# Kernel optimization log

Measured on AMD Instinct MI355X. Metric: run time of the kernel, lower is better.

## Reference

```python
import jax, jax.numpy as jnp
import numpy as np

B, T, D = 2, 2048, 1024
H = 16
HD = D // H
WINDOW = 128
N_GLOBAL = 1
SCALE = 1.0 / np.sqrt(HD)


def _attend_mask(T):
    # True = allowed to attend: banded local window + global rows/cols
    idx = jnp.arange(T)
    dist = jnp.abs(idx[:, None] - idx[None, :])
    attend = dist <= WINDOW
    glb = idx < N_GLOBAL
    attend = attend | glb[:, None] | glb[None, :]
    return attend  # [T, T] bool


def setup_inputs() -> dict:
    key = jax.random.key(0)
    ks = jax.random.split(key, 5)
    scale_w = 1.0 / np.sqrt(D)
    return {
        "x": jax.random.normal(ks[0], (B, T, D), dtype=jnp.float32),
        "Wq": jax.random.normal(ks[1], (D, D), dtype=jnp.float32) * scale_w,
        "Wk": jax.random.normal(ks[2], (D, D), dtype=jnp.float32) * scale_w,
        "Wv": jax.random.normal(ks[3], (D, D), dtype=jnp.float32) * scale_w,
        "Wo": jax.random.normal(ks[4], (D, D), dtype=jnp.float32) * scale_w,
    }


def reference(x, Wq, Wk, Wv, Wo):
    Bb, Tt, Dd = x.shape
    # torch nn.Linear: y = x @ W.T
    q = (x @ Wq.T).reshape(Bb, Tt, H, HD).transpose(0, 2, 1, 3)  # [B,H,T,hd]
    k = (x @ Wk.T).reshape(Bb, Tt, H, HD).transpose(0, 2, 1, 3)
    v = (x @ Wv.T).reshape(Bb, Tt, H, HD).transpose(0, 2, 1, 3)

    attend = _attend_mask(Tt)  # [T,T]
    logits = jnp.einsum("bhqd,bhkd->bhqk", q, k) * SCALE
    logits = jnp.where(attend[None, None, :, :], logits, -jnp.inf)
    weights = jax.nn.softmax(logits, axis=-1)
    weights = jnp.nan_to_num(weights)
    out = jnp.einsum("bhqk,bhkd->bhqd", weights, v)
    out = out.transpose(0, 2, 1, 3).reshape(Bb, Tt, Dd)
    return out @ Wo.T
```

## Files before the change

kernel.cpp:

```cpp
#include <hip/hip_runtime.h>

typedef unsigned short u16;
typedef __attribute__((ext_vector_type(8))) __bf16 bf16x8;
typedef __attribute__((ext_vector_type(4))) float f32x4;
typedef __attribute__((ext_vector_type(8))) u16 u16x8;

#define T_SEQ 2048
#define DIM   1024
#define HDIM  64
#define WIN   128
#define XN_EL (2 * T_SEQ * DIM)

#define AS1 __attribute__((address_space(1)))
#define AS3 __attribute__((address_space(3)))

__device__ __forceinline__ u16 f2bf(float f) {
  union { float f; unsigned u; } v; v.f = f;
  unsigned r = v.u + 0x7fffu + ((v.u >> 16) & 1u);
  return (u16)(r >> 16);
}
__device__ __forceinline__ float bf2f(u16 u) {
  union { unsigned u; float f; } v; v.u = ((unsigned)u) << 16; return v.f;
}
__device__ __forceinline__ void bar() {
  asm volatile("" ::: "memory");
  __builtin_amdgcn_s_barrier();
  asm volatile("" ::: "memory");
}

__global__ __launch_bounds__(256) void cvt_all(
    const float* __restrict__ x,  const float* __restrict__ wq,
    const float* __restrict__ wk, const float* __restrict__ wv,
    const float* __restrict__ wo, u16* __restrict__ xb, u16* __restrict__ wb) {
  const int bid = blockIdx.x;
  const float* s;
  u16* d;
  int off;
  if (bid < 2048) {
    s = x; d = xb; off = bid * 2048;
  } else {
    const int w = bid - 2048;
    const int m = w >> 9;
    s = (m == 0) ? wq : ((m == 1) ? wk : ((m == 2) ? wv : wo));
    d = wb + ((size_t)m << 20);
    off = (w & 511) * 2048;
  }
  const int i = off + threadIdx.x * 8;
  const float4* s4 = (const float4*)(s + i);
  float4 a = s4[0], b = s4[1];
  u16x8 r;
  r[0] = f2bf(a.x); r[1] = f2bf(a.y); r[2] = f2bf(a.z); r[3] = f2bf(a.w);
  r[4] = f2bf(b.x); r[5] = f2bf(b.y); r[6] = f2bf(b.z); r[7] = f2bf(b.w);
  *(u16x8*)(d + i) = r;
}

__global__ __launch_bounds__(512, 2) void gemm8(
    const u16* __restrict__ A, const u16* __restrict__ B,
    u16* __restrict__ C, int nbm) {
  constexpr int NT = 16;
  __shared__ u16 As[2][256 * 64];
  __shared__ u16 Bs[2][192 * 64];

  const int tid = threadIdx.x;
  const int lane = tid & 63;
  const int wid = tid >> 6;
  const int wr = wid >> 2, wc = wid & 3;
  const int c15 = lane & 15, g = lane >> 4;
  const int lr = lane >> 3;
  const int lcs = ((lane & 7) ^ lr) << 3;

  const int cpx = gridDim.x >> 3;
  const int bid = ((int)blockIdx.x & 7) * cpx + ((int)blockIdx.x >> 3);
  const int bm = bid % nbm;
  const int nb = bid / nbm;
  const u16* Ab = A + (size_t)bm * 256 * DIM;
  const u16* Bb = B + (size_t)nb * 192 * DIM;

  f32x4 acc[8][3];
#pragma unroll
  for (int m = 0; m < 8; ++m)
#pragma unroll
    for (int n = 0; n < 3; ++n) acc[m][n] = (f32x4){0.f, 0.f, 0.f, 0.f};

  auto stAh = [&](int buf, int half, int t) {
    const int k0 = t * 64;
#pragma unroll
    for (int i = 0; i < 2; ++i) {
      const int c = half * 16 + wid * 2 + i;
      __builtin_amdgcn_global_load_lds(
          (const AS1 void*)(Ab + (size_t)(c * 8 + lr) * DIM + k0 + lcs),
          (AS3 void*)(&As[buf][c * 512]), 16, 0, 0);
    }
  };
  auto stBt = [&](int buf, int third, int t) {
    const int k0 = t * 64;
    const int c = third * 8 + wid;
    __builtin_amdgcn_global_load_lds(
        (const AS1 void*)(Bb + (size_t)(c * 8 + lr) * DIM + k0 + lcs),
        (AS3 void*)(&Bs[buf][c * 512]), 16, 0, 0);
  };

  stAh(0, 0, 0); stAh(0, 1, 0);
  stBt(0, 0, 0); stBt(0, 1, 0); stBt(0, 2, 0);
  stBt(1, 0, 1); stBt(1, 1, 1); stBt(1, 2, 1);
  asm volatile("s_waitcnt vmcnt(3)" ::: "memory");
  bar();

  for (int t2 = 0; t2 < NT; t2 += 2) {
    bf16x8 bfrag[3][2];
#pragma unroll
    for (int p = 0; p < 8; ++p) {
      const int q = p & 3;
      const int buf = (p >> 2);
      if (q == 0) {
#pragma unroll
        for (int n = 0; n < 3; ++n)
#pragma unroll
          for (int ks = 0; ks < 2; ++ks) {
            const int r = wc * 48 + n * 16 + c15;
            bfrag[n][ks] = *(const bf16x8*)(
                &Bs[buf][r * 64 + ((ks * 32 + g * 8) ^ ((r & 7) << 3))]);
          }
      }
      bf16x8 af[2][2];
#pragma unroll
      for (int m = 0; m < 2; ++m)
#pragma unroll
        for (int ks = 0; ks < 2; ++ks) {
          const int r = wr * 128 + (q * 2 + m) * 16 + c15;
          af[m][ks] = *(const bf16x8*)(
              &As[buf][r * 64 + ((ks * 32 + g * 8) ^ ((r & 7) << 3))]);
        }
      const bool s2 = (t2 + 2) < NT;
      const bool s3 = (t2 + 3) < NT;
      if (p == 0) {
        stAh(1, 0, t2 + 1);
      } else if (p == 1) {
        stAh(1, 1, t2 + 1);
        if (s2) stBt(0, 0, t2 + 2);
      } else if (p == 2) {
        if (s2) stBt(0, 1, t2 + 2);
      } else if (p == 3) {
        if (s2) { stBt(0, 2, t2 + 2);
                  asm volatile("s_waitcnt vmcnt(3)" ::: "memory"); }
        else    { asm volatile("s_waitcnt vmcnt(0)" ::: "memory"); }
      } else if (p == 4) {
        if (s2) stAh(0, 0, t2 + 2);
      } else if (p == 5) {
        if (s2) stAh(0, 1, t2 + 2);
        if (s3) stBt(1, 0, t2 + 3);
      } else if (p == 6) {
        if (s3) stBt(1, 1, t2 + 3);
      } else {
        if (s3) { stBt(1, 2, t2 + 3);
                  asm volatile("s_waitcnt vmcnt(3)" ::: "memory"); }
        else if (s2) { asm volatile("s_waitcnt vmcnt(0)" ::: "memory"); }
      }
      bar();
      __builtin_amdgcn_s_setprio(1);
#pragma unroll
      for (int m = 0; m < 2; ++m)
#pragma unroll
        for (int n = 0; n < 3; ++n)
#pragma unroll
          for (int ks = 0; ks < 2; ++ks)
            acc[q * 2 + m][n] = __builtin_amdgcn_mfma_f32_16x16x32_bf16(
                af[m][ks], bfrag[n][ks], acc[q * 2 + m][n], 0, 0, 0);
      __builtin_amdgcn_s_setprio(0);
      bar();
    }
  }

#pragma unroll
  for (int m = 0; m < 8; ++m) {
    const int row0 = bm * 256 + wr * 128 + m * 16 + g * 4;
#pragma unroll
    for (int n = 0; n < 3; ++n) {
      const int col = nb * 192 + wc * 48 + n * 16 + c15;
#pragma unroll
      for (int j = 0; j < 4; ++j) {
        u16* dst = C + (size_t)(col >> 10) * (size_t)XN_EL +
                   (col & 1023) + (size_t)(row0 + j) * DIM;
        *dst = f2bf(acc[m][n][j]);
      }
    }
  }
}

template <int BM, int BN, int WM, int WN, int OS, typename OUT_T>
__global__ __launch_bounds__(WM * WN * 64, 2) void gemm3(
    const u16* __restrict__ A, const u16* __restrict__ B,
    OUT_T* __restrict__ C, int nbm) {
  constexpr int NW = WM * WN;
  constexpr int RM = BM / WM, RN = BN / WN;
  constexpr int MF = RM / 16, NF = RN / 16;
  constexpr int MPH = MF / 4;
  constexpr int NT = DIM / 64;
  constexpr int CA = BM / 8, CB = BN / 8;
  constexpr int ANW = CA / NW;
  constexpr int BNW = CB / NW;

  __shared__ u16 As[2][BM * 64];
  __shared__ u16 Bs[2][BN * 64];

  const int tid = threadIdx.x;
  const int lane = tid & 63;
  const int wid = tid >> 6;
  const int wr = wid / WN, wc = wid % WN;
  const int c15 = lane & 15, g = lane >> 4;
  const int lr = lane >> 3;
  const int lcs = ((lane & 7) ^ lr) << 3;

  const int cpx = gridDim.x >> 3;
  const int bid = ((int)blockIdx.x & 7) * cpx + ((int)blockIdx.x >> 3);
  const int bm = bid % nbm;
  const int nb = bid / nbm;
  const u16* Ab = A + (size_t)bm * BM * DIM;
  const u16* Bb = B + (size_t)nb * BN * DIM;

  f32x4 acc[MF][NF];
#pragma unroll
  for (int m = 0; m < MF; ++m)
#pragma unroll
    for (int n = 0; n < NF; ++n) acc[m][n] = (f32x4){0.f, 0.f, 0.f, 0.f};

  auto stA = [&](int buf, int half, int k0) {
#pragma unroll
    for (int i = 0; i < ANW / 2; ++i) {
      const int c = half * (CA / 2) + wid * (ANW / 2) + i;
      __builtin_amdgcn_global_load_lds(
          (const AS1 void*)(Ab + (size_t)(c * 8 + lr) * DIM + k0 + lcs),
          (AS3 void*)(&As[buf][c * 512]), 16, 0, 0);
    }
  };
  auto stB = [&](int buf, int k0) {
#pragma unroll
    for (int i = 0; i < BNW; ++i) {
      const int c = wid * BNW + i;
      __builtin_amdgcn_global_load_lds(
          (const AS1 void*)(Bb + (size_t)(c * 8 + lr) * DIM + k0 + lcs),
          (AS3 void*)(&Bs[buf][c * 512]), 16, 0, 0);
    }
  };

  stA(0, 0, 0); stA(0, 1, 0);
  stB(0, 0); stB(1, 64);
  asm volatile("s_waitcnt vmcnt(4)" ::: "memory");
  bar();

  for (int t = 0; t < NT; ++t) {
    const int buf = t & 1;
    const int k0 = t * 64;
    bf16x8 bfrag[NF][2];
#pragma unroll
    for (int p = 0; p < 4; ++p) {
      if (p == 0) {
#pragma unroll
        for (int n = 0; n < NF; ++n)
#pragma unroll
          for (int ks = 0; ks < 2; ++ks) {
            const int r = wc * RN + n * 16 + c15;
            bfrag[n][ks] = *(const bf16x8*)(
                &Bs[buf][r * 64 + ((ks * 32 + g * 8) ^ ((r & 7) << 3))]);
          }
      }
      bf16x8 af[MPH][2];
#pragma unroll
      for (int m = 0; m < MPH; ++m)
#pragma unroll
        for (int ks = 0; ks < 2; ++ks) {
          const int r = wr * RM + (p * MPH + m) * 16 + c15;
          af[m][ks] = *(const bf16x8*)(
              &As[buf][r * 64 + ((ks * 32 + g * 8) ^ ((r & 7) << 3))]);
        }
      if (p == 0) {
        if (t + 1 < NT) stA(buf ^ 1, 0, k0 + 64);
      } else if (p == 1) {
        if (t + 1 < NT) stA(buf ^ 1, 1, k0 + 64);
      } else if (p == 2) {
        if (t + 2 < NT) stB(buf, k0 + 128);
      } else {
        if (t < NT - 2) asm volatile("s_waitcnt vmcnt(4)" ::: "memory");
        else            asm volatile("s_waitcnt vmcnt(0)" ::: "memory");
      }
      bar();
      __builtin_amdgcn_s_setprio(1);
#pragma unroll
      for (int m = 0; m < MPH; ++m)
#pragma unroll
        for (int n = 0; n < NF; ++n)
#pragma unroll
          for (int ks = 0; ks < 2; ++ks)
            acc[p * MPH + m][n] = __builtin_amdgcn_mfma_f32_16x16x32_bf16(
                af[m][ks], bfrag[n][ks], acc[p * MPH + m][n], 0, 0, 0);
      __builtin_amdgcn_s_setprio(0);
      bar();
    }
  }

#pragma unroll
  for (int m = 0; m < MF; ++m) {
    const int row0 = bm * BM + wr * RM + m * 16 + g * 4;
#pragma unroll
    for (int n = 0; n < NF; ++n) {
      const int col = nb * BN + wc * RN + n * 16 + c15;
#pragma unroll
      for (int j = 0; j < 4; ++j) {
        const size_t idx = (size_t)(row0 + j) * OS + col;
        if constexpr (sizeof(OUT_T) == 2) C[idx] = f2bf(acc[m][n][j]);
        else C[idx] = acc[m][n][j];
      }
    }
  }
}

__global__ __launch_bounds__(256) void sparse_attn(
    const u16* __restrict__ Q, const u16* __restrict__ K,
    const u16* __restrict__ V, u16* __restrict__ AO) {
  __shared__ u16 Ks[64 * 72];
  __shared__ u16 Vt[64 * 72];
  __shared__ u16 Pl[4][16 * 72];
  __shared__ float Pg[4][32];

  const int tid = threadIdx.x;
  const int lane = tid & 63;
  const int wid = tid >> 6;
  const size_t ha = (size_t)blockIdx.z * T_SEQ * DIM + (size_t)blockIdx.y * HDIM;
  const u16* Qp = Q + ha;
  const u16* Kp = K + ha;
  const u16* Vp = V + ha;

  if (blockIdx.x == 16) {
    float* qs   = (float*)(&Pl[0][0]);
    float* ps   = (float*)Ks;
    float* rbuf = (float*)Vt;
    float* red  = (float*)Pg;

    if (tid < HDIM) qs[tid] = bf2f(Qp[tid]);
    __syncthreads();

    float lsum = 0.f;
#pragma unroll
    for (int j = 0; j < 8; ++j) {
      const int k = tid + 256 * j;
      const u16* kr = Kp + (size_t)k * DIM;
      float acc = 0.f;
#pragma unroll
      for (int d0 = 0; d0 < 8; ++d0) {
        u16x8 kv = *(const u16x8*)(kr + d0 * 8);
#pragma unroll
        for (int e = 0; e < 8; ++e) acc += qs[d0 * 8 + e] * bf2f(kv[e]);
      }
      const float p = __expf(acc * 0.125f);
      ps[k] = p;
      lsum += p;
    }
#pragma unroll
    for (int s = 1; s < 64; s <<= 1) lsum += __shfl_xor(lsum, s);
    if (lane == 0) red[wid] = lsum;
    __syncthreads();
    const float denom = red[0] + red[1] + red[2] + red[3];

    const int kg = tid >> 3, dg = tid & 7;
    float facc[8] = {0.f, 0.f, 0.f, 0.f, 0.f, 0.f, 0.f, 0.f};
#pragma unroll 8
    for (int i = 0; i < 64; ++i) {
      const int k = kg * 64 + i;
      const u16x8 vv = *(const u16x8*)(Vp + (size_t)k * DIM + dg * 8);
      const float p = ps[k];
#pragma unroll
      for (int e = 0; e < 8; ++e) facc[e] += p * bf2f(vv[e]);
    }
#pragma unroll
    for (int e = 0; e < 8; ++e) rbuf[kg * 64 + dg * 8 + e] = facc[e];
    __syncthreads();
    if (tid < HDIM) {
      float tot = 0.f;
#pragma unroll
      for (int k2 = 0; k2 < 32; ++k2) tot += rbuf[k2 * 64 + tid];
      AO[ha + tid] = f2bf(tot / denom);
    }
    return;
  }

  const int c15 = lane & 15;
  const int g = lane >> 4;
  const int q0 = blockIdx.x * 128;
  const int qw = q0 + wid * 32;

  bf16x8 qA0, qA1, qB0, qB1;
  {
    const u16* qp = Qp + (size_t)(qw + c15) * DIM + g * 8;
    qA0 = *(const bf16x8*)qp;
    qA1 = *(const bf16x8*)(qp + 32);
    const u16* qp2 = qp + 16 * DIM;
    qB0 = *(const bf16x8*)qp2;
    qB1 = *(const bf16x8*)(qp2 + 32);
  }

  float lrA[4] = {0.f, 0.f, 0.f, 0.f}, lrB[4] = {0.f, 0.f, 0.f, 0.f};
  f32x4 aoA[4], aoB[4];
#pragma unroll
  for (int c = 0; c < 4; ++c) {
    aoA[c] = (f32x4){0.f, 0.f, 0.f, 0.f};
    aoB[c] = (f32x4){0.f, 0.f, 0.f, 0.f};
  }

  const int klo = (q0 > WIN) ? (q0 - WIN) : 0;
  int khi = q0 + 128 + WIN;
  if (khi > T_SEQ) khi = T_SEQ;
  const int nt = (khi - klo) >> 6;

  const int srr = tid >> 2;
  const int scc = (tid & 3) * 16;
  const int vr = srr ^ (scc & 48);

  const u16* kbase = Kp + (size_t)(klo + srr) * DIM + scc;
  const u16* vbase = Vp + (size_t)(klo + srr) * DIM + scc;
  u16x8 kp0 = *(const u16x8*)kbase;
  u16x8 kp1 = *(const u16x8*)(kbase + 8);
  u16x8 vp0 = *(const u16x8*)vbase;
  u16x8 vp1 = *(const u16x8*)(vbase + 8);

  for (int ti = 0; ti < nt; ++ti) {
    const int kt = klo + ti * 64;
    *(u16x8*)(Ks + srr * 72 + scc) = kp0;
    *(u16x8*)(Ks + srr * 72 + scc + 8) = kp1;
#pragma unroll
    for (int e = 0; e < 8; ++e) {
      Vt[(scc + e) * 72 + vr] = vp0[e];
      Vt[(scc + 8 + e) * 72 + vr] = vp1[e];
    }
    __syncthreads();

    if (ti + 1 < nt) {
      const u16* kn = kbase + (size_t)(ti + 1) * 64 * DIM;
      const u16* vn = vbase + (size_t)(ti + 1) * 64 * DIM;
      kp0 = *(const u16x8*)kn;
      kp1 = *(const u16x8*)(kn + 8);
      vp0 = *(const u16x8*)vn;
      vp1 = *(const u16x8*)(vn + 8);
    }

    auto do_group = [&](const bf16x8& qf0, const bf16x8& qf1, int r0,
                        float* lrun, f32x4* ao) {
      f32x4 s[4];
#pragma unroll
      for (int t = 0; t < 4; ++t) {
        const u16* kr = Ks + (t * 16 + c15) * 72 + g * 8;
        bf16x8 ka = *(const bf16x8*)kr;
        bf16x8 kb = *(const bf16x8*)(kr + 32);
        f32x4 z = (f32x4){0.f, 0.f, 0.f, 0.f};
        z = __builtin_amdgcn_mfma_f32_16x16x32_bf16(qf0, ka, z, 0, 0, 0);
        s[t] = __builtin_amdgcn_mfma_f32_16x16x32_bf16(qf1, kb, z, 0, 0, 0);
      }
      if (kt >= r0 - 113 && kt <= r0 + 65) {
#pragma unroll
        for (int j = 0; j < 4; ++j) {
#pragma unroll
          for (int t = 0; t < 4; ++t) {
            const float p = __expf(s[t][j] * 0.125f);
            lrun[j] += p;
            Pl[wid][(g * 4 + j) * 72 + t * 16 + c15] = f2bf(p);
          }
        }
      } else {
#pragma unroll
        for (int j = 0; j < 4; ++j) {
          const int qg = r0 + g * 4 + j;
#pragma unroll
          for (int t = 0; t < 4; ++t) {
            const int kg = kt + t * 16 + c15;
            const int dd = qg - kg;
            const bool ok = (kg == 0) || (dd <= WIN && dd >= -WIN);
            const float p = ok ? __expf(s[t][j] * 0.125f) : 0.f;
            lrun[j] += p;
            Pl[wid][(g * 4 + j) * 72 + t * 16 + c15] = f2bf(p);
          }
        }
      }
      asm volatile("s_waitcnt lgkmcnt(0)" ::: "memory");

      const bf16x8 pa0 = *(const bf16x8*)(&Pl[wid][c15 * 72 + g * 8]);
      const bf16x8 pa1 = *(const bf16x8*)(&Pl[wid][c15 * 72 + 32 + g * 8]);
#pragma unroll
      for (int c = 0; c < 4; ++c) {
        const int rb = (c * 16 + c15) * 72;
        bf16x8 va = *(const bf16x8*)(Vt + rb + ((g * 8) ^ (c << 4)));
        bf16x8 vb = *(const bf16x8*)(Vt + rb + ((32 + g * 8) ^ (c << 4)));
        ao[c] = __builtin_amdgcn_mfma_f32_16x16x32_bf16(pa0, va, ao[c], 0, 0, 0);
        ao[c] = __builtin_amdgcn_mfma_f32_16x16x32_bf16(pa1, vb, ao[c], 0, 0, 0);
      }
    };

    do_group(qA0, qA1, qw, lrA, aoA);
    do_group(qB0, qB1, qw + 16, lrB, aoB);

    __syncthreads();
  }

  float ltA[4], ltB[4];
#pragma unroll
  for (int j = 0; j < 4; ++j) {
    float a = lrA[j], b = lrB[j];
    a += __shfl_xor(a, 1); b += __shfl_xor(b, 1);
    a += __shfl_xor(a, 2); b += __shfl_xor(b, 2);
    a += __shfl_xor(a, 4); b += __shfl_xor(b, 4);
    a += __shfl_xor(a, 8); b += __shfl_xor(b, 8);
    ltA[j] = a; ltB[j] = b;
  }

  if (klo > 0) {
    const u16x8 k0a = *(const u16x8*)(Kp + g * 8);
    const u16x8 k0b = *(const u16x8*)(Kp + 32 + g * 8);
    const u16x8 qa0 = *(const u16x8*)&qA0;
    const u16x8 qa1 = *(const u16x8*)&qA1;
    const u16x8 qb0 = *(const u16x8*)&qB0;
    const u16x8 qb1 = *(const u16x8*)&qB1;
    float sgA = 0.f, sgB = 0.f;
#pragma unroll
    for (int e = 0; e < 8; ++e) {
      sgA += bf2f(qa0[e]) * bf2f(k0a[e]) + bf2f(qa1[e]) * bf2f(k0b[e]);
      sgB += bf2f(qb0[e]) * bf2f(k0a[e]) + bf2f(qb1[e]) * bf2f(k0b[e]);
    }
    sgA += __shfl_xor(sgA, 16); sgA += __shfl_xor(sgA, 32);
    sgB += __shfl_xor(sgB, 16); sgB += __shfl_xor(sgB, 32);
    Pg[wid][c15] = __expf(sgA * 0.125f);
    Pg[wid][16 + c15] = __expf(sgB * 0.125f);
    asm volatile("s_waitcnt lgkmcnt(0)" ::: "memory");
#pragma unroll
    for (int j = 0; j < 4; ++j) {
      const float pA = Pg[wid][g * 4 + j];
      const float pB = Pg[wid][16 + g * 4 + j];
      ltA[j] += pA;
      ltB[j] += pB;
#pragma unroll
      for (int c = 0; c < 4; ++c) {
        const float v0 = bf2f(Vp[c * 16 + c15]);
        aoA[c][j] += pA * v0;
        aoB[c][j] += pB * v0;
      }
    }
  }

#pragma unroll
  for (int j = 0; j < 4; ++j) {
    const int qrA = qw + g * 4 + j;
    const int qrB = qrA + 16;
    const float invA = 1.0f / ltA[j];
    const float invB = 1.0f / ltB[j];
#pragma unroll
    for (int c = 0; c < 4; ++c) {
      if (qrA != 0)
        AO[ha + (size_t)qrA * DIM + c * 16 + c15] = f2bf(aoA[c][j] * invA);
      AO[ha + (size_t)qrB * DIM + c * 16 + c15] = f2bf(aoB[c][j] * invB);
    }
  }
}

extern "C" void kernel_launch(void* const* d_in, const int* in_sizes, int n_in,
                              void* d_out, int out_size, void* d_ws, size_t ws_size,
                              hipStream_t stream) {
  const float* x  = (const float*)d_in[0];
  const float* Wq = (const float*)d_in[1];
  const float* Wk = (const float*)d_in[2];
  const float* Wv = (const float*)d_in[3];
  const float* Wo = (const float*)d_in[4];
  float* out = (float*)d_out;

  const int WN = DIM * DIM;

  u16* ws  = (u16*)d_ws;
  u16* xb  = ws;
  u16* wb  = ws + (size_t)XN_EL;
  u16* Wob = wb + (size_t)3 * WN;
  u16* Qb  = wb + (size_t)4 * WN;
  u16* Kb  = Qb + (size_t)XN_EL;
  u16* Vb  = Kb + (size_t)XN_EL;

  cvt_all<<<4096, 256, 0, stream>>>(x, Wq, Wk, Wv, Wo, xb, wb);

  gemm8<<<256, 512, 0, stream>>>(xb, wb, Qb, 16);

  sparse_attn<<<dim3(17, 16, 2), 256, 0, stream>>>(Qb, Kb, Vb, xb);

  gemm3<128, 128, 2, 2, DIM, float><<<256, 256, 0, stream>>>(xb, Wob, out, 32);
}
```

Baseline: 102.4 us.

## Stage full K/V window in LDS upfront and move global-row block first

The attention kernel now loads the entire key/value window (up to 384 rows) into shared memory before the compute loop, replacing the per-tile load/store with two barriers per iteration by a single barrier. The global-query block is moved from the last block index to block 0, so the long serial global row starts first instead of trailing. The change removes per-tile synchronisation stalls, at the cost of much larger LDS use (about 105 KB), which limits occupancy to roughly one block per CU and removes overlap of loads with compute.

After: 108.8 us. 6.3% more time.

```diff
diff --git a/kernel.cpp b/kernel.cpp
--- a/kernel.cpp
+++ b/kernel.cpp
@@ -10,6 +10,7 @@
 #define HDIM  64
 #define WIN   128
 #define XN_EL (2 * T_SEQ * DIM)
+#define VP    392
 
 #define AS1 __attribute__((address_space(1)))
 #define AS3 __attribute__((address_space(3)))
@@ -317,8 +318,8 @@
 __global__ __launch_bounds__(256) void sparse_attn(
     const u16* __restrict__ Q, const u16* __restrict__ K,
     const u16* __restrict__ V, u16* __restrict__ AO) {
-  __shared__ u16 Ks[64 * 72];
-  __shared__ u16 Vt[64 * 72];
+  __shared__ u16 Ks[384 * 72];
+  __shared__ u16 Vt[64 * VP];
   __shared__ u16 Pl[4][16 * 72];
   __shared__ float Pg[4][32];
 
@@ -330,7 +331,7 @@
   const u16* Kp = K + ha;
   const u16* Vp = V + ha;
 
-  if (blockIdx.x == 16) {
+  if (blockIdx.x == 0) {
     float* qs   = (float*)(&Pl[0][0]);
     float* ps   = (float*)Ks;
     float* rbuf = (float*)Vt;
@@ -385,7 +386,7 @@
 
   const int c15 = lane & 15;
   const int g = lane >> 4;
-  const int q0 = blockIdx.x * 128;
+  const int q0 = (blockIdx.x - 1) * 128;
   const int qw = q0 + wid * 32;
 
   bf16x8 qA0, qA1, qB0, qB1;
@@ -398,61 +399,63 @@
     qB1 = *(const bf16x8*)(qp2 + 32);
   }
 
-  float lrA[4] = {0.f, 0.f, 0.f, 0.f}, lrB[4] = {0.f, 0.f, 0.f, 0.f};
-  f32x4 aoA[4], aoB[4];
-#pragma unroll
-  for (int c = 0; c < 4; ++c) {
-    aoA[c] = (f32x4){0.f, 0.f, 0.f, 0.f};
-    aoB[c] = (f32x4){0.f, 0.f, 0.f, 0.f};
-  }
-
   const int klo = (q0 > WIN) ? (q0 - WIN) : 0;
   int khi = q0 + 128 + WIN;
   if (khi > T_SEQ) khi = T_SEQ;
   const int nt = (khi - klo) >> 6;
 
-  const int srr = tid >> 2;
-  const int scc = (tid & 3) * 16;
-  const int vr = srr ^ (scc & 48);
-
-  const u16* kbase = Kp + (size_t)(klo + srr) * DIM + scc;
-  const u16* vbase = Vp + (size_t)(klo + srr) * DIM + scc;
-  u16x8 kp0 = *(const u16x8*)kbase;
-  u16x8 kp1 = *(const u16x8*)(kbase + 8);
-  u16x8 vp0 = *(const u16x8*)vbase;
-  u16x8 vp1 = *(const u16x8*)(vbase + 8);
+  {
+    const int srr = tid >> 2;
+    const int scc = (tid & 3) * 16;
+    const int vsw = srr ^ (scc & 48);
+    const u16* kb = Kp + (size_t)(klo + srr) * DIM + scc;
+    const u16* vb = Vp + (size_t)(klo + srr) * DIM + scc;
+    u16x8 k0 = *(const u16x8*)kb, k1 = *(const u16x8*)(kb + 8);
+    u16x8 v0 = *(const u16x8*)vb, v1 = *(const u16x8*)(vb + 8);
+    for (int tt = 0; tt < nt; ++tt) {
+      u16x8 ck0 = k0, ck1 = k1, cv0 = v0, cv1 = v1;
+      if (tt + 1 < nt) {
+        const u16* kn = kb + (size_t)(tt + 1) * 64 * DIM;
+        const u16* vn = vb + (size_t)(tt + 1) * 64 * DIM;
+        k0 = *(const u16x8*)kn; k1 = *(const u16x8*)(kn + 8);
+        v0 = *(const u16x8*)vn; v1 = *(const u16x8*)(vn + 8);
+      }
+      const int lr = tt * 64 + srr;
+      *(u16x8*)(Ks + lr * 72 + scc) = ck0;
+      *(u16x8*)(Ks + lr * 72 + scc + 8) = ck1;
+      const int vc = tt * 64 + vsw;
+#pragma unroll
+      for (int e = 0; e < 8; ++e) {
+        Vt[(scc + e) * VP + vc] = cv0[e];
+        Vt[(scc + 8 + e) * VP + vc] = cv1[e];
+      }
+    }
+  }
+  __syncthreads();
+
+  float lrA[4] = {0.f, 0.f, 0.f, 0.f}, lrB[4] = {0.f, 0.f, 0.f, 0.f};
+  f32x4 aoA[4], aoB[4];
+#pragma unroll
+  for (int c = 0; c < 4; ++c) {
+    aoA[c] = (f32x4){0.f, 0.f, 0.f, 0.f};
+    aoB[c] = (f32x4){0.f, 0.f, 0.f, 0.f};
+  }
 
   for (int ti = 0; ti < nt; ++ti) {
     const int kt = klo + ti * 64;
-    *(u16x8*)(Ks + srr * 72 + scc) = kp0;
-    *(u16x8*)(Ks + srr * 72 + scc + 8) = kp1;
-#pragma unroll
-    for (int e = 0; e < 8; ++e) {
-      Vt[(scc + e) * 72 + vr] = vp0[e];
-      Vt[(scc + 8 + e) * 72 + vr] = vp1[e];
-    }
-    __syncthreads();
-
-    if (ti + 1 < nt) {
-      const u16* kn = kbase + (size_t)(ti + 1) * 64 * DIM;
-      const u16* vn = vbase + (size_t)(ti + 1) * 64 * DIM;
-      kp0 = *(const u16x8*)kn;
-      kp1 = *(const u16x8*)(kn + 8);
-      vp0 = *(const u16x8*)vn;
-      vp1 = *(const u16x8*)(vn + 8);
-    }
+    const int tb = ti * 64;
 
     auto do_group = [&](const bf16x8& qf0, const bf16x8& qf1, int r0,
                         float* lrun, f32x4* ao) {
       f32x4 s[4];
 #pragma unroll
       for (int t = 0; t < 4; ++t) {
-        const u16* kr = Ks + (t * 16 + c15) * 72 + g * 8;
+        const u16* kr = Ks + (size_t)(tb + t * 16 + c15) * 72 + g * 8;
         bf16x8 ka = *(const bf16x8*)kr;
-        bf16x8 kb = *(const bf16x8*)(kr + 32);
+        bf16x8 kb2 = *(const bf16x8*)(kr + 32);
         f32x4 z = (f32x4){0.f, 0.f, 0.f, 0.f};
         z = __builtin_amdgcn_mfma_f32_16x16x32_bf16(qf0, ka, z, 0, 0, 0);
-        s[t] = __builtin_amdgcn_mfma_f32_16x16x32_bf16(qf1, kb, z, 0, 0, 0);
+        s[t] = __builtin_amdgcn_mfma_f32_16x16x32_bf16(qf1, kb2, z, 0, 0, 0);
       }
       if (kt >= r0 - 113 && kt <= r0 + 65) {
 #pragma unroll
@@ -485,18 +488,16 @@
       const bf16x8 pa1 = *(const bf16x8*)(&Pl[wid][c15 * 72 + 32 + g * 8]);
 #pragma unroll
       for (int c = 0; c < 4; ++c) {
-        const int rb = (c * 16 + c15) * 72;
-        bf16x8 va = *(const bf16x8*)(Vt + rb + ((g * 8) ^ (c << 4)));
-        bf16x8 vb = *(const bf16x8*)(Vt + rb + ((32 + g * 8) ^ (c << 4)));
+        const int rb = (c * 16 + c15) * VP;
+        bf16x8 va = *(const bf16x8*)(Vt + rb + tb + ((g * 8) ^ (c << 4)));
+        bf16x8 vb2 = *(const bf16x8*)(Vt + rb + tb + ((32 + g * 8) ^ (c << 4)));
         ao[c] = __builtin_amdgcn_mfma_f32_16x16x32_bf16(pa0, va, ao[c], 0, 0, 0);
-        ao[c] = __builtin_amdgcn_mfma_f32_16x16x32_bf16(pa1, vb, ao[c], 0, 0, 0);
+        ao[c] = __builtin_amdgcn_mfma_f32_16x16x32_bf16(pa1, vb2, ao[c], 0, 0, 0);
       }
     };
 
     do_group(qA0, qA1, qw, lrA, aoA);
     do_group(qB0, qB1, qw + 16, lrB, aoB);
-
-    __syncthreads();
   }
 
   float ltA[4], ltB[4];
```
